# Kernel tuning notes

Measured on AMD Instinct MI355X. Metric: run time of the kernel, lower is better.

## Reference

```python
import jax, jax.numpy as jnp
import numpy as np

EPS = 1e-6  # model.epsilon


def setup_inputs() -> dict:
    key = jax.random.key(0)
    k1, k2 = jax.random.split(key)
    # X: one-hot-like translated sequence tensor [genomes, tiles, 6 frames, tile_len, alphabet]
    X = jax.random.uniform(k1, (8, 12, 6, 2000, 21), dtype=jnp.float32)
    Q = jnp.full((21,), 1.0 / 21.0, dtype=jnp.float32)  # background aa distribution
    # P_logit initialized like log(Q) + noise (matches _getRandomProfiles)
    P_logit = jnp.log(Q)[None, :, None] + 4.0 * jax.random.normal(k2, (8, 21, 48), dtype=jnp.float32)
    return {"X": X, "P_logit": P_logit, "Q": Q}


def reference(X, P_logit, Q):
    # P = softmax over alphabet axis; R = log odds vs background, clamped at epsilon
    P = jax.nn.softmax(P_logit, axis=1)                      # [k, A, U]
    R = jnp.log(jnp.maximum(P / Q[None, :, None], EPS))      # [k, A, U]
    D0, D1, D2, L, A = X.shape
    k, _, U = R.shape
    # conv2d with spatial (L, A), in_ch 1, out_ch U; width window covers full alphabet
    Xr = X.reshape(D0 * D1 * D2, L, A, 1)
    W = R.reshape(k, A, 1, U)
    Z = jax.lax.conv_general_dilated(
        Xr, W, window_strides=(1, 1), padding='VALID',
        dimension_numbers=('NHWC', 'HWIO', 'NHWC'))          # [B, L-k+1, 1, U]
    Z = Z.reshape(D0, D1, D2, L - k + 1, U)                  # [D0, D1, D2, P, U]
    S = jnp.max(Z, axis=(2, 3))                              # max over frames & positions -> [D0, D1, U]
    return (S, R, Z)
```

## Files before the change

### kernel.cpp

```cpp
#include <hip/hip_runtime.h>
#include <math.h>

typedef __attribute__((ext_vector_type(8))) short short8;
typedef __attribute__((ext_vector_type(4))) float f32x4;

#define D0n 8
#define D1n 12
#define D2n 6
#define Ln 2000
#define An 21
#define KPn 8
#define Un 48
#define PPn 1993
#define Bn 576
#define S_SIZE 4608
#define R_SIZE 8064

#define BPn 256
#define TILES 4
#define XROWS 264
#define XBUF_BYTES (XROWS * 64)
#define RB_BYTES (384 * 64)
#define BOFF (2 * XBUF_BYTES)
#define RED_OFF (BOFF + RB_BYTES)

__device__ __forceinline__ int swz(int b) { return b ^ ((b >> 2) & 0x70); }

__device__ __forceinline__ unsigned int fkey(float f) {
    unsigned int u = __float_as_uint(f);
    return (u & 0x80000000u) ? ~u : (u | 0x80000000u);
}
__device__ __forceinline__ float funkey(unsigned int k) {
    return __uint_as_float((k & 0x80000000u) ? (k ^ 0x80000000u) : ~k);
}
__device__ __forceinline__ unsigned short f2bf(float v) {
    unsigned int b = __float_as_uint(v);
    return (unsigned short)((b + 0x7FFFu + ((b >> 16) & 1u)) >> 16);
}

#define GLOAD_LDS16(g, l)                                                     \
    __builtin_amdgcn_global_load_lds(                                          \
        (const __attribute__((address_space(1))) void*)(g),                    \
        (__attribute__((address_space(3))) void*)(l), 16, 0, 0)

__global__ void k_profile(const float* __restrict__ P_logit,
                          const float* __restrict__ Q,
                          float* __restrict__ Rout,
                          unsigned short* __restrict__ Rb,
                          unsigned int* __restrict__ Skey) {
    int t = blockIdx.x * blockDim.x + threadIdx.x;
    if (t < S_SIZE) Skey[t] = 0u;
    if (t >= KPn * Un) return;
    int kp = t / Un, u = t % Un;
    const float* pl = P_logit + kp * (An * Un) + u;
    float v[An];
    float m = -INFINITY;
#pragma unroll
    for (int a = 0; a < An; ++a) { v[a] = pl[a * Un]; m = fmaxf(m, v[a]); }
    float s = 0.f;
#pragma unroll
    for (int a = 0; a < An; ++a) { v[a] = expf(v[a] - m); s += v[a]; }
    float inv = 1.f / s;
    int rowp = kp * Un + u;
#pragma unroll
    for (int a = 0; a < An; ++a) {
        float r = logf(fmaxf(v[a] * inv / Q[a], 1e-6f));
        Rout[(kp * An + a) * Un + u] = r;
        Rb[swz(rowp * 64 + a * 2) >> 1] = f2bf(r);
    }
#pragma unroll
    for (int a = An; a < 32; ++a) Rb[swz(rowp * 64 + a * 2) >> 1] = 0;
}

__device__ __forceinline__ void xwrite4(char* xbase, int idx, f32x4 g) {
    int fi = idx * 4;
    int row = fi / An;
    int a = fi - row * An;
#pragma unroll
    for (int e = 0; e < 4; ++e) {
        *(unsigned short*)(xbase + swz(row * 64 + a * 2)) = f2bf(g[e]);
        ++a;
        if (a == An) { a = 0; ++row; }
    }
}

__global__ __launch_bounds__(512) void k_conv(
        const float* __restrict__ X,
        const unsigned short* __restrict__ Rb,
        float* __restrict__ Z,
        unsigned int* __restrict__ Skey) {
    __shared__ char smem[2 * XBUF_BYTES + RB_BYTES + 8 * Un * 4];
    const int b = blockIdx.y;
    const int base_p = blockIdx.x * (TILES * BPn);
    const int t = threadIdx.x;
    const int w = t >> 6;
    const int l = t & 63;
    const int lr = l & 15;
    const int ls = l >> 4;
    const int pw = w * 32;

    {
        const uint4* src = (const uint4*)Rb;
        uint4* dst = (uint4*)(smem + BOFF);
#pragma unroll
        for (int i = 0; i < RB_BYTES / 16 / 512; ++i) {
            int idx = t + i * 512;
            GLOAD_LDS16(src + idx, dst + idx);
        }
    }
    {
        uint4 z4 = {0u, 0u, 0u, 0u};
        uint4* xs = (uint4*)smem;
        for (int i = t; i < 2 * XBUF_BYTES / 16; i += 512) xs[i] = z4;
    }
    const float* Xb = X + ((size_t)b * Ln + base_p) * An;
    f32x4 g[3];
    int n4_0;
    {
        int rows = min(XROWS, Ln - base_p);
        n4_0 = rows * An / 4;
        const f32x4* src = (const f32x4*)Xb;
#pragma unroll
        for (int i = 0; i < 3; ++i) {
            int idx = t + i * 512;
            g[i] = (idx < n4_0) ? src[idx] : (f32x4){0.f, 0.f, 0.f, 0.f};
        }
    }
    __syncthreads();
#pragma unroll
    for (int i = 0; i < 3; ++i) {
        int idx = t + i * 512;
        if (idx < n4_0) xwrite4((char*)smem, idx, g[i]);
    }
    __syncthreads();

    float smax[3][4];
#pragma unroll
    for (int nu = 0; nu < 3; ++nu)
#pragma unroll
        for (int r = 0; r < 4; ++r) smax[nu][r] = -INFINITY;

    int n4_next = 0;
    for (int tt = 0; tt < TILES; ++tt) {
        char* xb = (char*)smem + (tt & 1) * XBUF_BYTES;
        const int tp0 = base_p + tt * BPn;

        if (tt + 1 < TILES) {
            int np0 = base_p + (tt + 1) * BPn;
            int rows = min(XROWS, Ln - np0);
            n4_next = rows * An / 4;
            const f32x4* src = (const f32x4*)(X + ((size_t)b * Ln + np0) * An);
#pragma unroll
            for (int i = 0; i < 3; ++i) {
                int idx = t + i * 512;
                g[i] = (idx < n4_next) ? src[idx] : (f32x4){0.f, 0.f, 0.f, 0.f};
            }
        }

        f32x4 acc[3][2];
#pragma unroll
        for (int nu = 0; nu < 3; ++nu)
#pragma unroll
            for (int np = 0; np < 2; ++np) acc[nu][np] = (f32x4){0.f, 0.f, 0.f, 0.f};

#pragma unroll
        for (int q = 0; q < KPn; ++q) {
            const int rr = q * Un + lr;
            short8 rf0 = *(const short8*)(smem + BOFF + swz(rr * 64 + ls * 16));
            short8 rf1 = *(const short8*)(smem + BOFF + swz((rr + 16) * 64 + ls * 16));
            short8 rf2 = *(const short8*)(smem + BOFF + swz((rr + 32) * 64 + ls * 16));
            const int xr = pw + q + lr;
            short8 xf0 = *(const short8*)(xb + swz(xr * 64 + ls * 16));
            short8 xf1 = *(const short8*)(xb + swz((xr + 16) * 64 + ls * 16));
            acc[0][0] = __builtin_amdgcn_mfma_f32_16x16x32_bf16(rf0, xf0, acc[0][0], 0, 0, 0);
            acc[0][1] = __builtin_amdgcn_mfma_f32_16x16x32_bf16(rf0, xf1, acc[0][1], 0, 0, 0);
            acc[1][0] = __builtin_amdgcn_mfma_f32_16x16x32_bf16(rf1, xf0, acc[1][0], 0, 0, 0);
            acc[1][1] = __builtin_amdgcn_mfma_f32_16x16x32_bf16(rf1, xf1, acc[1][1], 0, 0, 0);
            acc[2][0] = __builtin_amdgcn_mfma_f32_16x16x32_bf16(rf2, xf0, acc[2][0], 0, 0, 0);
            acc[2][1] = __builtin_amdgcn_mfma_f32_16x16x32_bf16(rf2, xf1, acc[2][1], 0, 0, 0);
        }

#pragma unroll
        for (int np = 0; np < 2; ++np) {
            int p = tp0 + pw + np * 16 + lr;
            if (p < PPn) {
                float* zp = Z + ((size_t)b * PPn + p) * Un + ls * 4;
#pragma unroll
                for (int nu = 0; nu < 3; ++nu) {
                    *(f32x4*)(zp + nu * 16) = acc[nu][np];
#pragma unroll
                    for (int r = 0; r < 4; ++r)
                        smax[nu][r] = fmaxf(smax[nu][r], acc[nu][np][r]);
                }
            }
        }

        if (tt + 1 < TILES) {
            __syncthreads();
            char* xn = (char*)smem + ((tt + 1) & 1) * XBUF_BYTES;
#pragma unroll
            for (int i = 0; i < 3; ++i) {
                int idx = t + i * 512;
                if (idx < n4_next) xwrite4(xn, idx, g[i]);
            }
            __syncthreads();
        }
    }

    float* red = (float*)(smem + RED_OFF);
#pragma unroll
    for (int nu = 0; nu < 3; ++nu)
#pragma unroll
        for (int r = 0; r < 4; ++r) {
            float v = smax[nu][r];
            v = fmaxf(v, __shfl_xor(v, 1));
            v = fmaxf(v, __shfl_xor(v, 2));
            v = fmaxf(v, __shfl_xor(v, 4));
            v = fmaxf(v, __shfl_xor(v, 8));
            if (lr == 0) red[w * Un + nu * 16 + ls * 4 + r] = v;
        }
    __syncthreads();
    if (t < Un) {
        float m = -INFINITY;
#pragma unroll
        for (int wv = 0; wv < 8; ++wv) m = fmaxf(m, red[wv * Un + t]);
        atomicMax(&Skey[(b / D2n) * Un + t], fkey(m));
    }
}

__global__ void k_decode(unsigned int* __restrict__ Skey) {
    int t = blockIdx.x * blockDim.x + threadIdx.x;
    if (t < S_SIZE) {
        float f = funkey(Skey[t]);
        ((float*)Skey)[t] = f;
    }
}

extern "C" void kernel_launch(void* const* d_in, const int* in_sizes, int n_in,
                              void* d_out, int out_size, void* d_ws, size_t ws_size,
                              hipStream_t stream) {
    const float* X = (const float*)d_in[0];
    const float* P_logit = (const float*)d_in[1];
    const float* Q = (const float*)d_in[2];

    float* S = (float*)d_out;
    float* Rout = S + S_SIZE;
    float* Z = Rout + R_SIZE;
    unsigned short* Rb = (unsigned short*)d_ws;

    k_profile<<<(S_SIZE + 63) / 64, 64, 0, stream>>>(P_logit, Q, Rout, Rb,
                                                     (unsigned int*)d_out);

    dim3 grid(2, Bn);
    k_conv<<<grid, 512, 0, stream>>>(X, Rb, Z, (unsigned int*)d_out);

    k_decode<<<(S_SIZE + 255) / 256, 256, 0, stream>>>((unsigned int*)d_out);
}
```

Before: 88.34 us.

## Split conv into more blocks with two tiles each and restructured pipeline

Result: faster. 82.53 us (-6.6%).

```diff
diff --git a/kernel.cpp b/kernel.cpp
--- a/kernel.cpp
+++ b/kernel.cpp
@@ -17,7 +17,8 @@
 #define R_SIZE 8064
 
 #define BPn 256
-#define TILES 4
+#define TILES 2
+#define NBX 4
 #define XROWS 264
 #define XBUF_BYTES (XROWS * 64)
 #define RB_BYTES (384 * 64)
@@ -42,6 +43,13 @@
     __builtin_amdgcn_global_load_lds(                                          \
         (const __attribute__((address_space(1))) void*)(g),                    \
         (__attribute__((address_space(3))) void*)(l), 16, 0, 0)
+
+#define TILE_BARRIER()                                                        \
+    do {                                                                      \
+        asm volatile("s_waitcnt lgkmcnt(0)" ::: "memory");                    \
+        __builtin_amdgcn_s_barrier();                                         \
+        asm volatile("" ::: "memory");                                        \
+    } while (0)
 
 __global__ void k_profile(const float* __restrict__ P_logit,
                           const float* __restrict__ Q,
@@ -84,12 +92,74 @@
     }
 }
 
-__global__ __launch_bounds__(512) void k_conv(
+__device__ __forceinline__ void xload(const float* __restrict__ X, int b,
+                                      int tp0, int t, f32x4 g[3], int& n4) {
+    int rows = min(XROWS, Ln - tp0);
+    n4 = rows * An / 4;
+    const f32x4* src = (const f32x4*)(X + ((size_t)b * Ln + tp0) * An);
+#pragma unroll
+    for (int i = 0; i < 3; ++i) {
+        int idx = t + i * 512;
+        g[i] = (idx < n4) ? src[idx] : (f32x4){0.f, 0.f, 0.f, 0.f};
+    }
+}
+
+__device__ __forceinline__ void xstore(char* xbase, int t, const f32x4 g[3],
+                                       int n4) {
+#pragma unroll
+    for (int i = 0; i < 3; ++i) {
+        int idx = t + i * 512;
+        if (idx < n4) xwrite4(xbase, idx, g[i]);
+    }
+}
+
+__device__ __forceinline__ void qloop8(const char* smem, const char* xb,
+                                       int lr, int ls, int pw,
+                                       f32x4 acc[3][2]) {
+#pragma unroll
+    for (int q = 0; q < KPn; ++q) {
+        const int rr = q * Un + lr;
+        short8 rf0 = *(const short8*)(smem + BOFF + swz(rr * 64 + ls * 16));
+        short8 rf1 = *(const short8*)(smem + BOFF + swz((rr + 16) * 64 + ls * 16));
+        short8 rf2 = *(const short8*)(smem + BOFF + swz((rr + 32) * 64 + ls * 16));
+        const int xr = pw + q + lr;
+        short8 xf0 = *(const short8*)(xb + swz(xr * 64 + ls * 16));
+        short8 xf1 = *(const short8*)(xb + swz((xr + 16) * 64 + ls * 16));
+        acc[0][0] = __builtin_amdgcn_mfma_f32_16x16x32_bf16(rf0, xf0, acc[0][0], 0, 0, 0);
+        acc[0][1] = __builtin_amdgcn_mfma_f32_16x16x32_bf16(rf0, xf1, acc[0][1], 0, 0, 0);
+        acc[1][0] = __builtin_amdgcn_mfma_f32_16x16x32_bf16(rf1, xf0, acc[1][0], 0, 0, 0);
+        acc[1][1] = __builtin_amdgcn_mfma_f32_16x16x32_bf16(rf1, xf1, acc[1][1], 0, 0, 0);
+        acc[2][0] = __builtin_amdgcn_mfma_f32_16x16x32_bf16(rf2, xf0, acc[2][0], 0, 0, 0);
+        acc[2][1] = __builtin_amdgcn_mfma_f32_16x16x32_bf16(rf2, xf1, acc[2][1], 0, 0, 0);
+    }
+}
+
+__device__ __forceinline__ void store_tile(float* __restrict__ Z, int b,
+                                           int tp0, int pw, int lr, int ls,
+                                           const f32x4 acc[3][2],
+                                           float smax[3][4]) {
+#pragma unroll
+    for (int np = 0; np < 2; ++np) {
+        int p = tp0 + pw + np * 16 + lr;
+        if (p < PPn) {
+            float* zp = Z + ((size_t)b * PPn + p) * Un + ls * 4;
+#pragma unroll
+            for (int nu = 0; nu < 3; ++nu) {
+                *(f32x4*)(zp + nu * 16) = acc[nu][np];
+#pragma unroll
+                for (int r = 0; r < 4; ++r)
+                    smax[nu][r] = fmaxf(smax[nu][r], acc[nu][np][r]);
+            }
+        }
+    }
+}
+
+__global__ __launch_bounds__(512, 4) void k_conv(
         const float* __restrict__ X,
         const unsigned short* __restrict__ Rb,
         float* __restrict__ Z,
         unsigned int* __restrict__ Skey) {
-    __shared__ char smem[2 * XBUF_BYTES + RB_BYTES + 8 * Un * 4];
+    __shared__ char smem[RED_OFF + 8 * Un * 4];
     const int b = blockIdx.y;
     const int base_p = blockIdx.x * (TILES * BPn);
     const int t = threadIdx.x;
@@ -113,26 +183,12 @@
         uint4* xs = (uint4*)smem;
         for (int i = t; i < 2 * XBUF_BYTES / 16; i += 512) xs[i] = z4;
     }
-    const float* Xb = X + ((size_t)b * Ln + base_p) * An;
     f32x4 g[3];
-    int n4_0;
-    {
-        int rows = min(XROWS, Ln - base_p);
-        n4_0 = rows * An / 4;
-        const f32x4* src = (const f32x4*)Xb;
-#pragma unroll
-        for (int i = 0; i < 3; ++i) {
-            int idx = t + i * 512;
-            g[i] = (idx < n4_0) ? src[idx] : (f32x4){0.f, 0.f, 0.f, 0.f};
-        }
-    }
+    int n4;
+    xload(X, b, base_p, t, g, n4);
     __syncthreads();
-#pragma unroll
-    for (int i = 0; i < 3; ++i) {
-        int idx = t + i * 512;
-        if (idx < n4_0) xwrite4((char*)smem, idx, g[i]);
-    }
-    __syncthreads();
+    xstore((char*)smem, t, g, n4);
+    TILE_BARRIER();
 
     float smax[3][4];
 #pragma unroll
@@ -140,72 +196,24 @@
 #pragma unroll
         for (int r = 0; r < 4; ++r) smax[nu][r] = -INFINITY;
 
-    int n4_next = 0;
-    for (int tt = 0; tt < TILES; ++tt) {
-        char* xb = (char*)smem + (tt & 1) * XBUF_BYTES;
-        const int tp0 = base_p + tt * BPn;
-
-        if (tt + 1 < TILES) {
-            int np0 = base_p + (tt + 1) * BPn;
-            int rows = min(XROWS, Ln - np0);
-            n4_next = rows * An / 4;
-            const f32x4* src = (const f32x4*)(X + ((size_t)b * Ln + np0) * An);
-#pragma unroll
-            for (int i = 0; i < 3; ++i) {
-                int idx = t + i * 512;
-                g[i] = (idx < n4_next) ? src[idx] : (f32x4){0.f, 0.f, 0.f, 0.f};
-            }
-        }
-
-        f32x4 acc[3][2];
-#pragma unroll
-        for (int nu = 0; nu < 3; ++nu)
-#pragma unroll
-            for (int np = 0; np < 2; ++np) acc[nu][np] = (f32x4){0.f, 0.f, 0.f, 0.f};
-
-#pragma unroll
-        for (int q = 0; q < KPn; ++q) {
-            const int rr = q * Un + lr;
-            short8 rf0 = *(const short8*)(smem + BOFF + swz(rr * 64 + ls * 16));
-            short8 rf1 = *(const short8*)(smem + BOFF + swz((rr + 16) * 64 + ls * 16));
-            short8 rf2 = *(const short8*)(smem + BOFF + swz((rr + 32) * 64 + ls * 16));
-            const int xr = pw + q + lr;
-            short8 xf0 = *(const short8*)(xb + swz(xr * 64 + ls * 16));
-            short8 xf1 = *(const short8*)(xb + swz((xr + 16) * 64 + ls * 16));
-            acc[0][0] = __builtin_amdgcn_mfma_f32_16x16x32_bf16(rf0, xf0, acc[0][0], 0, 0, 0);
-            acc[0][1] = __builtin_amdgcn_mfma_f32_16x16x32_bf16(rf0, xf1, acc[0][1], 0, 0, 0);
-            acc[1][0] = __builtin_amdgcn_mfma_f32_16x16x32_bf16(rf1, xf0, acc[1][0], 0, 0, 0);
-            acc[1][1] = __builtin_amdgcn_mfma_f32_16x16x32_bf16(rf1, xf1, acc[1][1], 0, 0, 0);
-            acc[2][0] = __builtin_amdgcn_mfma_f32_16x16x32_bf16(rf2, xf0, acc[2][0], 0, 0, 0);
-            acc[2][1] = __builtin_amdgcn_mfma_f32_16x16x32_bf16(rf2, xf1, acc[2][1], 0, 0, 0);
-        }
-
-#pragma unroll
-        for (int np = 0; np < 2; ++np) {
-            int p = tp0 + pw + np * 16 + lr;
-            if (p < PPn) {
-                float* zp = Z + ((size_t)b * PPn + p) * Un + ls * 4;
-#pragma unroll
-                for (int nu = 0; nu < 3; ++nu) {
-                    *(f32x4*)(zp + nu * 16) = acc[nu][np];
-#pragma unroll
-                    for (int r = 0; r < 4; ++r)
-                        smax[nu][r] = fmaxf(smax[nu][r], acc[nu][np][r]);
-                }
-            }
-        }
-
-        if (tt + 1 < TILES) {
-            __syncthreads();
-            char* xn = (char*)smem + ((tt + 1) & 1) * XBUF_BYTES;
-#pragma unroll
-            for (int i = 0; i < 3; ++i) {
-                int idx = t + i * 512;
-                if (idx < n4_next) xwrite4(xn, idx, g[i]);
-            }
-            __syncthreads();
-        }
-    }
+    f32x4 acc[3][2];
+
+    xload(X, b, base_p + BPn, t, g, n4);
+#pragma unroll
+    for (int nu = 0; nu < 3; ++nu)
+#pragma unroll
+        for (int np = 0; np < 2; ++np) acc[nu][np] = (f32x4){0.f, 0.f, 0.f, 0.f};
+    qloop8((const char*)smem, (const char*)smem, lr, ls, pw, acc);
+    xstore((char*)smem + XBUF_BYTES, t, g, n4);
+    store_tile(Z, b, base_p, pw, lr, ls, acc, smax);
+    TILE_BARRIER();
+
+#pragma unroll
+    for (int nu = 0; nu < 3; ++nu)
+#pragma unroll
+        for (int np = 0; np < 2; ++np) acc[nu][np] = (f32x4){0.f, 0.f, 0.f, 0.f};
+    qloop8((const char*)smem, (const char*)smem + XBUF_BYTES, lr, ls, pw, acc);
+    store_tile(Z, b, base_p + BPn, pw, lr, ls, acc, smax);
 
     float* red = (float*)(smem + RED_OFF);
 #pragma unroll
@@ -251,7 +259,7 @@
     k_profile<<<(S_SIZE + 63) / 64, 64, 0, stream>>>(P_logit, Q, Rout, Rb,
                                                      (unsigned int*)d_out);
 
-    dim3 grid(2, Bn);
+    dim3 grid(NBX, Bn);
     k_conv<<<grid, 512, 0, stream>>>(X, Rb, Z, (unsigned int*)d_out);
 
     k_decode<<<(S_SIZE + 255) / 256, 256, 0, stream>>>((unsigned int*)d_out);
```
